# Performance work log

Hardware: AMD Instinct MI355X
Metric: run time of the kernel (lower is better)

Reference implementation:

```python
import jax, jax.numpy as jnp
import numpy as np

DIM = 256
HEADS = 8
PS = 8  # patch/window size
EPS = 1e-5


def _ln(x, g, b):
    m = x.mean(-1, keepdims=True)
    v = x.var(-1, keepdims=True)
    return (x - m) / jnp.sqrt(v + EPS) * g + b


def setup_inputs() -> dict:
    key = jax.random.key(0)
    ks = jax.random.split(key, 10)
    B, C, H, W = 4, DIM, 256, 256
    s = 0.02
    return {
        "y_lf": jax.random.normal(ks[0], (B, C, H, W), jnp.float32),
        "y_hf": jax.random.normal(ks[1], (B, C, H, W), jnp.float32),
        "g_lf": jnp.ones((C,), jnp.float32),
        "b_lf": jnp.zeros((C,), jnp.float32),
        "g_hf": jnp.ones((C,), jnp.float32),
        "b_hf": jnp.zeros((C,), jnp.float32),
        "Wq": jax.random.normal(ks[2], (C, C), jnp.float32) * s,
        "bq": jnp.zeros((C,), jnp.float32),
        "Wk": jax.random.normal(ks[3], (C, C), jnp.float32) * s,
        "bk": jnp.zeros((C,), jnp.float32),
        "Wv": jax.random.normal(ks[4], (C, C), jnp.float32) * s,
        "bv": jnp.zeros((C,), jnp.float32),
        "Wo": jax.random.normal(ks[5], (C, C), jnp.float32) * s,
        "bo": jnp.zeros((C,), jnp.float32),
    }


def reference(y_lf, y_hf, g_lf, b_lf, g_hf, b_hf, Wq, bq, Wk, bk, Wv, bv, Wo, bo):
    B, C, H, W = y_lf.shape
    ps = PS
    hd = C // HEADS
    nH, nW = H // ps, W // ps

    def win_tokens(x):
        # (B,C,H,W) -> (B*nH*nW, ps*ps, C)
        x = x.reshape(B, C, nH, ps, nW, ps)
        return x.transpose(0, 2, 4, 3, 5, 1).reshape(-1, ps * ps, C)

    lf = win_tokens(y_lf)
    hf = win_tokens(y_hf)  # residual + V source (un-normalized, as in torch code)

    q = _ln(lf, g_lf, b_lf) @ Wq.T + bq
    k = _ln(hf, g_hf, b_hf) @ Wk.T + bk
    v = hf @ Wv.T + bv

    BW, L, _ = q.shape
    q = q.reshape(BW, L, HEADS, hd)
    k = k.reshape(BW, L, HEADS, hd)
    v = v.reshape(BW, L, HEADS, hd)

    scale = 1.0 / np.sqrt(hd).astype(np.float32)
    scores = jnp.einsum('bqhd,bkhd->bhqk', q, k) * scale
    attn = jax.nn.softmax(scores, axis=-1)
    o = jnp.einsum('bhqk,bkhd->bqhd', attn, v).reshape(BW, L, C)
    o = o @ Wo.T + bo + hf  # out_proj + residual

    # window_reverse: (B*nH*nW, ps*ps, C) -> (B,C,H,W)
    o = o.reshape(B, nH, nW, ps, ps, C)
    o = o.transpose(0, 5, 1, 3, 2, 4).reshape(B, C, H, W)
    return o
```

## Files before the change

### kernel.cpp

```cpp
#include <hip/hip_runtime.h>

typedef float  f4     __attribute__((ext_vector_type(4)));
typedef float  f32x4  __attribute__((ext_vector_type(4)));
typedef short  short8 __attribute__((ext_vector_type(8)));
typedef __bf16 bf16x8 __attribute__((ext_vector_type(8)));
typedef int    int4v  __attribute__((ext_vector_type(4)));
typedef unsigned short us4 __attribute__((ext_vector_type(4)));

__device__ __forceinline__ unsigned short f2bf(float f) {
    unsigned int u = __builtin_bit_cast(unsigned int, f);
    u += 0x7FFFu + ((u >> 16) & 1u);
    return (unsigned short)(u >> 16);
}
__device__ __forceinline__ float bf2f(unsigned short h) {
    unsigned int u = ((unsigned int)h) << 16;
    return __builtin_bit_cast(float, u);
}
__device__ __forceinline__ f32x4 mfma_bf16(short8 a, short8 b, f32x4 c) {
    return __builtin_amdgcn_mfma_f32_16x16x32_bf16(
        __builtin_bit_cast(bf16x8, a), __builtin_bit_cast(bf16x8, b), c, 0, 0, 0);
}
__device__ __forceinline__ int cvt_pk_bf16(float lo, float hi) {
    int d;
    asm volatile("v_cvt_pk_bf16_f32 %0, %1, %2" : "=v"(d) : "v"(lo), "v"(hi));
    return d;
}
__device__ __forceinline__ int bperm(int addr, int src) {
    return __builtin_amdgcn_ds_bpermute(addr, src);
}

__global__ void pcaf_precvt(const float* __restrict__ Wq, const float* __restrict__ bq,
                            const float* __restrict__ Wk, const float* __restrict__ bk,
                            const float* __restrict__ Wv, const float* __restrict__ Wo,
                            const float* __restrict__ g_lf, const float* __restrict__ b_lf,
                            const float* __restrict__ g_hf, const float* __restrict__ b_hf,
                            void* __restrict__ ws) {
    const int mat  = blockIdx.x >> 8;
    const int row  = blockIdx.x & 255;
    const int lane = threadIdx.x;
    const float* W = (mat == 0) ? Wq : (mat == 1) ? Wk : (mat == 2) ? Wv : Wo;
    f4 w = *(const f4*)(W + row * 256 + lane * 4);
    f4 wp = w;
    if (mat < 2) {
        const float* g = mat ? g_hf : g_lf;
        f4 gg = *(const f4*)(g + lane * 4);
        wp = w * gg;
    }
    us4 u;
    u[0] = f2bf(wp[0]); u[1] = f2bf(wp[1]); u[2] = f2bf(wp[2]); u[3] = f2bf(wp[3]);
    *(us4*)((unsigned short*)ws + mat * 65536 + row * 256 + lane * 4) = u;
    if (mat < 2) {
        const float* b = mat ? b_hf : b_lf;
        f4 bb = *(const f4*)(b + lane * 4);
        float rsum = wp[0] + wp[1] + wp[2] + wp[3];
        float cb   = bb[0] * w[0] + bb[1] * w[1] + bb[2] * w[2] + bb[3] * w[3];
        #pragma unroll
        for (int d = 1; d < 64; d <<= 1) {
            rsum += __shfl_xor(rsum, d);
            cb   += __shfl_xor(cb, d);
        }
        if (lane == 0) {
            float* cons = (float*)((char*)ws + 524288);
            cons[mat * 512 + row]       = rsum;
            cons[mat * 512 + 256 + row] = cb + (mat ? bk[row] : bq[row]);
        }
    }
}

struct AccW { f32x4 a[4][2]; };

__device__ __forceinline__ AccW gemmW(const char* sm, int off,
                                      const unsigned short* __restrict__ Wb,
                                      int c0, int g, int l15) {
    AccW r;
    f32x4 z = {0.f, 0.f, 0.f, 0.f};
    #pragma unroll
    for (int m = 0; m < 4; ++m) { r.a[m][0] = z; r.a[m][1] = z; }
    #pragma unroll
    for (int half = 0; half < 2; ++half) {
        short8 w0[4], w1[4];
        #pragma unroll
        for (int k = 0; k < 4; ++k) {
            w0[k] = *(const short8*)(Wb + c0 * 256 + (half * 4 + k) * 32 + g * 8);
            w1[k] = *(const short8*)(Wb + (c0 + 16) * 256 + (half * 4 + k) * 32 + g * 8);
        }
        #pragma unroll
        for (int k = 0; k < 4; ++k) {
            #pragma unroll
            for (int m = 0; m < 4; ++m) {
                short8 am = *(const short8*)(sm + off + (16 * m + l15) * 528 +
                                             ((half * 4 + k) * 32 + g * 8) * 2);
                r.a[m][0] = mfma_bf16(am, w0[k], r.a[m][0]);
                r.a[m][1] = mfma_bf16(am, w1[k], r.a[m][1]);
            }
        }
    }
    return r;
}

__global__ __attribute__((amdgpu_flat_work_group_size(512, 512), amdgpu_waves_per_eu(4, 4)))
void pcaf4_kernel(
    const float* __restrict__ y_lf, const float* __restrict__ y_hf,
    const float* __restrict__ bv, const float* __restrict__ bo,
    const void* __restrict__ ws, float* __restrict__ out)
{
    constexpr int C = 256, H = 256, W = 256, HW = H * W;
    constexpr int RS = 528;
    constexpr int OA = 0;
    constexpr int OB = 33792;
    constexpr int OS = 67584;
    __shared__ __align__(16) char sm[68608];

    const unsigned short* wsq = (const unsigned short*)ws;
    const unsigned short* wsk = wsq + 65536;
    const unsigned short* wsv = wsq + 131072;
    const unsigned short* wso = wsq + 196608;
    const float* cons = (const float*)((const char*)ws + 524288);

    const int tid = threadIdx.x;
    const int bid = blockIdx.x;
    const int wi  = ((bid & 7) << 9) | (bid >> 3);
    const int bb  = wi >> 10;
    const int nh  = (wi >> 5) & 31;
    const int nw  = wi & 31;
    const long win_base = (long)bb * C * HW + (long)(nh * 8) * W + nw * 8;

    const int wave = tid >> 6;
    const int lane = tid & 63;
    const int g    = lane >> 4;
    const int l15  = lane & 15;
    const int c0   = 32 * wave + l15;

    {
        f4 lv[8], hv[8];
        #pragma unroll
        for (int it = 0; it < 4; ++it) {
            int q2  = it * 512 + tid;
            int c2  = q2 >> 4;
            int ph  = (q2 >> 1) & 7;
            int pw4 = (q2 & 1) * 4;
            long go = win_base + (long)(2 * c2) * HW + ph * W + pw4;
            lv[2 * it]     = *(const f4*)(y_lf + go);
            lv[2 * it + 1] = *(const f4*)(y_lf + go + HW);
            hv[2 * it]     = *(const f4*)(y_hf + go);
            hv[2 * it + 1] = *(const f4*)(y_hf + go + HW);
        }
        #pragma unroll
        for (int it = 0; it < 4; ++it) {
            int q2  = it * 512 + tid;
            int c2  = q2 >> 4;
            int ph  = (q2 >> 1) & 7;
            int pw4 = (q2 & 1) * 4;
            int tok0 = ph * 8 + pw4;
            #pragma unroll
            for (int j = 0; j < 4; ++j) {
                unsigned int lvv = (unsigned int)f2bf(lv[2 * it][j]) | ((unsigned int)f2bf(lv[2 * it + 1][j]) << 16);
                unsigned int hvv = (unsigned int)f2bf(hv[2 * it][j]) | ((unsigned int)f2bf(hv[2 * it + 1][j]) << 16);
                *(unsigned int*)(sm + OA + (tok0 + j) * RS + c2 * 4) = lvv;
                *(unsigned int*)(sm + OB + (tok0 + j) * RS + c2 * 4) = hvv;
            }
        }
    }
    __syncthreads();

    {
        const int t = tid >> 3, j = tid & 7;
        #pragma unroll
        for (int pass = 0; pass < 2; ++pass) {
            const int base = pass ? OB : OA;
            float sum = 0.f, ss = 0.f;
            #pragma unroll
            for (int r = 0; r < 4; ++r) {
                short8 raw = *(const short8*)(sm + base + t * RS + (j * 32 + r * 8) * 2);
                #pragma unroll
                for (int e = 0; e < 8; ++e) { float f = bf2f((unsigned short)raw[e]); sum += f; ss += f * f; }
            }
            sum += __shfl_xor(sum, 1); ss += __shfl_xor(ss, 1);
            sum += __shfl_xor(sum, 2); ss += __shfl_xor(ss, 2);
            sum += __shfl_xor(sum, 4); ss += __shfl_xor(ss, 4);
            float mean = sum * (1.f / 256.f);
            float rstd = rsqrtf(ss * (1.f / 256.f) - mean * mean + 1e-5f);
            if (j == 0) {
                float* S = (float*)(sm + OS);
                S[pass * 128 + t]      = mean;
                S[pass * 128 + 64 + t] = rstd;
            }
        }
    }

    AccW qacc = gemmW(sm, OA, wsq, c0, g, l15);

    unsigned int resp[4][2][2];
    #pragma unroll
    for (int m = 0; m < 4; ++m)
        #pragma unroll
        for (int n = 0; n < 2; ++n)
            #pragma unroll
            for (int jh = 0; jh < 2; ++jh) {
                unsigned int lo = *(const unsigned short*)(sm + OB + (16 * m + 4 * g + 2 * jh) * RS + (c0 + 16 * n) * 2);
                unsigned int hi = *(const unsigned short*)(sm + OB + (16 * m + 4 * g + 2 * jh + 1) * RS + (c0 + 16 * n) * 2);
                resp[m][n][jh] = lo | (hi << 16);
            }

    int vp[4][2][2];
    {
        AccW vacc = gemmW(sm, OB, wsv, c0, g, l15);
        float bv0 = bv[c0], bv1 = bv[c0 + 16];
        #pragma unroll
        for (int m = 0; m < 4; ++m) {
            vp[m][0][0] = cvt_pk_bf16(vacc.a[m][0][0] + bv0, vacc.a[m][0][1] + bv0);
            vp[m][0][1] = cvt_pk_bf16(vacc.a[m][0][2] + bv0, vacc.a[m][0][3] + bv0);
            vp[m][1][0] = cvt_pk_bf16(vacc.a[m][1][0] + bv1, vacc.a[m][1][1] + bv1);
            vp[m][1][1] = cvt_pk_bf16(vacc.a[m][1][2] + bv1, vacc.a[m][1][3] + bv1);
        }
    }
    __syncthreads();

    {
        const float* S = (const float*)(sm + OS);
        const float SCALE = 0.17677669529663687f;
        float rs0 = cons[c0], rs1 = cons[c0 + 16];
        float cb0 = cons[256 + c0], cb1 = cons[256 + c0 + 16];
        #pragma unroll
        for (int m = 0; m < 4; ++m)
            #pragma unroll
            for (int i = 0; i < 4; ++i) {
                int t = 16 * m + 4 * g + i;
                float mean = S[t], rstd = S[64 + t];
                float v0 = (rstd * (qacc.a[m][0][i] - mean * rs0) + cb0) * SCALE;
                float v1 = (rstd * (qacc.a[m][1][i] - mean * rs1) + cb1) * SCALE;
                *(unsigned short*)(sm + OA + t * RS + c0 * 2)        = f2bf(v0);
                *(unsigned short*)(sm + OA + t * RS + (c0 + 16) * 2) = f2bf(v1);
            }
    }

    AccW kacc = gemmW(sm, OB, wsk, c0, g, l15);
    __syncthreads();

    {
        const float* S = (const float*)(sm + OS);
        float rs0 = cons[512 + c0], rs1 = cons[512 + c0 + 16];
        float cb0 = cons[768 + c0], cb1 = cons[768 + c0 + 16];
        #pragma unroll
        for (int m = 0; m < 4; ++m)
            #pragma unroll
            for (int i = 0; i < 4; ++i) {
                int t = 16 * m + 4 * g + i;
                float mean = S[128 + t], rstd = S[192 + t];
                float v0 = rstd * (kacc.a[m][0][i] - mean * rs0) + cb0;
                float v1 = rstd * (kacc.a[m][1][i] - mean * rs1) + cb1;
                *(unsigned short*)(sm + OB + t * RS + c0 * 2)        = f2bf(v0);
                *(unsigned short*)(sm + OB + t * RS + (c0 + 16) * 2) = f2bf(v1);
            }
    }
    __syncthreads();

    {
        const int w = wave;
        short8 kf[4], qf[4];
        #pragma unroll
        for (int x = 0; x < 4; ++x) {
            kf[x] = *(const short8*)(sm + OB + (16 * x + l15) * RS + (32 * w + 8 * g) * 2);
            qf[x] = *(const short8*)(sm + OA + (16 * x + l15) * RS + (32 * w + 8 * g) * 2);
        }
        __syncthreads();

        f32x4 z = {0.f, 0.f, 0.f, 0.f};

        const int a0 = ((2 * (g & 1)) * 16 + l15) * 4;
        const int a1 = a0 + 64;
        const bool ghi = (g >> 1) & 1;

        short8 vf[2][2];
        #pragma unroll
        for (int kk = 0; kk < 2; ++kk)
            #pragma unroll
            for (int n2 = 0; n2 < 2; ++n2) {
                int4v t;
                #pragma unroll
                for (int j = 0; j < 4; ++j) {
                    int ad = (j >> 1) ? a1 : a0;
                    int v0 = bperm(ad, vp[2 * kk][n2][j & 1]);
                    int v1 = bperm(ad, vp[2 * kk + 1][n2][j & 1]);
                    t[j] = ghi ? v1 : v0;
                }
                vf[kk][n2] = __builtin_bit_cast(short8, t);
            }

        f32x4 o[4][2];
        #pragma unroll
        for (int c = 0; c < 4; ++c) { o[c][0] = z; o[c][1] = z; }

        #pragma unroll
        for (int c = 0; c < 4; ++c) {
            f32x4 stc[4];
            #pragma unroll
            for (int nk = 0; nk < 4; ++nk)
                stc[nk] = mfma_bf16(kf[nk], qf[c], z);

            float mx = stc[0][0];
            #pragma unroll
            for (int nk = 0; nk < 4; ++nk)
                #pragma unroll
                for (int i = 0; i < 4; ++i) mx = fmaxf(mx, stc[nk][i]);
            mx = fmaxf(mx, __shfl_xor(mx, 16));
            mx = fmaxf(mx, __shfl_xor(mx, 32));
            float sum = 0.f;
            #pragma unroll
            for (int nk = 0; nk < 4; ++nk)
                #pragma unroll
                for (int i = 0; i < 4; ++i) {
                    float e = __expf(stc[nk][i] - mx);
                    stc[nk][i] = e;
                    sum += e;
                }
            sum += __shfl_xor(sum, 16);
            sum += __shfl_xor(sum, 32);
            float is = 1.f / sum;

            int p[4][2];
            #pragma unroll
            for (int nk = 0; nk < 4; ++nk) {
                p[nk][0] = cvt_pk_bf16(stc[nk][0] * is, stc[nk][1] * is);
                p[nk][1] = cvt_pk_bf16(stc[nk][2] * is, stc[nk][3] * is);
            }

            #pragma unroll
            for (int kk = 0; kk < 2; ++kk) {
                int4v t;
                #pragma unroll
                for (int j = 0; j < 4; ++j) {
                    int ad = (j >> 1) ? a1 : a0;
                    int v0 = bperm(ad, p[2 * kk][j & 1]);
                    int v1 = bperm(ad, p[2 * kk + 1][j & 1]);
                    t[j] = ghi ? v1 : v0;
                }
                short8 pf = __builtin_bit_cast(short8, t);
                o[c][0] = mfma_bf16(pf, vf[kk][0], o[c][0]);
                o[c][1] = mfma_bf16(pf, vf[kk][1], o[c][1]);
            }
        }

        #pragma unroll
        for (int c = 0; c < 4; ++c)
            #pragma unroll
            for (int i = 0; i < 4; ++i) {
                int t = 16 * c + 4 * g + i;
                *(unsigned short*)(sm + OA + t * RS + c0 * 2)        = f2bf(o[c][0][i]);
                *(unsigned short*)(sm + OA + t * RS + (c0 + 16) * 2) = f2bf(o[c][1][i]);
            }
    }
    __syncthreads();

    {
        AccW oacc = gemmW(sm, OA, wso, c0, g, l15);
        float bo0 = bo[c0], bo1 = bo[c0 + 16];
        #pragma unroll
        for (int n = 0; n < 2; ++n) {
            float bon = n ? bo1 : bo0;
            int cout = c0 + 16 * n;
            #pragma unroll
            for (int m = 0; m < 4; ++m) {
                int tok0 = 16 * m + 4 * g;
                int ph = tok0 >> 3, pw = tok0 & 7;
                f4 ov;
                #pragma unroll
                for (int i = 0; i < 4; ++i) {
                    float rv = bf2f((unsigned short)((resp[m][n][i >> 1] >> (16 * (i & 1))) & 0xFFFF));
                    ov[i] = oacc.a[m][n][i] + bon + rv;
                }
                *(f4*)(out + win_base + (long)cout * HW + ph * W + pw) = ov;
            }
        }
    }
}

extern "C" void kernel_launch(void* const* d_in, const int* in_sizes, int n_in,
                              void* d_out, int out_size, void* d_ws, size_t ws_size,
                              hipStream_t stream) {
    (void)in_sizes; (void)n_in; (void)out_size; (void)ws_size;
    const float* y_lf = (const float*)d_in[0];
    const float* y_hf = (const float*)d_in[1];
    const float* g_lf = (const float*)d_in[2];
    const float* b_lf = (const float*)d_in[3];
    const float* g_hf = (const float*)d_in[4];
    const float* b_hf = (const float*)d_in[5];
    const float* Wq   = (const float*)d_in[6];
    const float* bq   = (const float*)d_in[7];
    const float* Wk   = (const float*)d_in[8];
    const float* bk   = (const float*)d_in[9];
    const float* Wv   = (const float*)d_in[10];
    const float* bv   = (const float*)d_in[11];
    const float* Wo   = (const float*)d_in[12];
    const float* bo   = (const float*)d_in[13];
    float* out = (float*)d_out;

    pcaf_precvt<<<dim3(1024), dim3(64), 0, stream>>>(
        Wq, bq, Wk, bk, Wv, Wo, g_lf, b_lf, g_hf, b_hf, d_ws);
    pcaf4_kernel<<<dim3(4096), dim3(512), 0, stream>>>(
        y_lf, y_hf, bv, bo, d_ws, out);
}
```

Before: 513.5 us.

## Pre-swizzle bf16 weights into MFMA fragment order and change LDS row stride

```diff
diff --git a/kernel.cpp b/kernel.cpp
--- a/kernel.cpp
+++ b/kernel.cpp
@@ -48,7 +48,16 @@
     }
     us4 u;
     u[0] = f2bf(wp[0]); u[1] = f2bf(wp[1]); u[2] = f2bf(wp[2]); u[3] = f2bf(wp[3]);
-    *(us4*)((unsigned short*)ws + mat * 65536 + row * 256 + lane * 4) = u;
+    {
+        const int ct   = row >> 4;
+        const int l15r = row & 15;
+        const int k_   = lane >> 3;
+        const int g_   = (lane >> 1) & 3;
+        const int e4   = (lane & 1) * 4;
+        unsigned short* dst = (unsigned short*)ws + mat * 65536 +
+                              (((ct * 8 + k_) * 64) + g_ * 16 + l15r) * 8 + e4;
+        *(us4*)dst = u;
+    }
     if (mat < 2) {
         const float* b = mat ? b_hf : b_lf;
         f4 bb = *(const f4*)(b + lane * 4);
@@ -67,11 +76,13 @@
     }
 }
 
+constexpr int RS = 536;
+
 struct AccW { f32x4 a[4][2]; };
 
 __device__ __forceinline__ AccW gemmW(const char* sm, int off,
-                                      const unsigned short* __restrict__ Wb,
-                                      int c0, int g, int l15) {
+                                      const unsigned short* __restrict__ Wbw,
+                                      int lane, int g, int l15) {
     AccW r;
     f32x4 z = {0.f, 0.f, 0.f, 0.f};
     #pragma unroll
@@ -81,14 +92,14 @@
         short8 w0[4], w1[4];
         #pragma unroll
         for (int k = 0; k < 4; ++k) {
-            w0[k] = *(const short8*)(Wb + c0 * 256 + (half * 4 + k) * 32 + g * 8);
-            w1[k] = *(const short8*)(Wb + (c0 + 16) * 256 + (half * 4 + k) * 32 + g * 8);
+            w0[k] = *(const short8*)(Wbw + (half * 4 + k) * 512 + lane * 8);
+            w1[k] = *(const short8*)(Wbw + 4096 + (half * 4 + k) * 512 + lane * 8);
         }
         #pragma unroll
         for (int k = 0; k < 4; ++k) {
             #pragma unroll
             for (int m = 0; m < 4; ++m) {
-                short8 am = *(const short8*)(sm + off + (16 * m + l15) * 528 +
+                short8 am = *(const short8*)(sm + off + (16 * m + l15) * RS +
                                              ((half * 4 + k) * 32 + g * 8) * 2);
                 r.a[m][0] = mfma_bf16(am, w0[k], r.a[m][0]);
                 r.a[m][1] = mfma_bf16(am, w1[k], r.a[m][1]);
@@ -99,17 +110,16 @@
 }
 
 __global__ __attribute__((amdgpu_flat_work_group_size(512, 512), amdgpu_waves_per_eu(4, 4)))
-void pcaf4_kernel(
+void pcaf5_kernel(
     const float* __restrict__ y_lf, const float* __restrict__ y_hf,
     const float* __restrict__ bv, const float* __restrict__ bo,
     const void* __restrict__ ws, float* __restrict__ out)
 {
     constexpr int C = 256, H = 256, W = 256, HW = H * W;
-    constexpr int RS = 528;
     constexpr int OA = 0;
-    constexpr int OB = 33792;
-    constexpr int OS = 67584;
-    __shared__ __align__(16) char sm[68608];
+    constexpr int OB = 34304;
+    constexpr int OS = 68608;
+    __shared__ __align__(16) char sm[69632];
 
     const unsigned short* wsq = (const unsigned short*)ws;
     const unsigned short* wsk = wsq + 65536;
@@ -188,7 +198,7 @@
         }
     }
 
-    AccW qacc = gemmW(sm, OA, wsq, c0, g, l15);
+    AccW qacc = gemmW(sm, OA, wsq + wave * 8192, lane, g, l15);
 
     unsigned int resp[4][2][2];
     #pragma unroll
@@ -204,7 +214,7 @@
 
     int vp[4][2][2];
     {
-        AccW vacc = gemmW(sm, OB, wsv, c0, g, l15);
+        AccW vacc = gemmW(sm, OB, wsv + wave * 8192, lane, g, l15);
         float bv0 = bv[c0], bv1 = bv[c0 + 16];
         #pragma unroll
         for (int m = 0; m < 4; ++m) {
@@ -234,7 +244,7 @@
             }
     }
 
-    AccW kacc = gemmW(sm, OB, wsk, c0, g, l15);
+    AccW kacc = gemmW(sm, OB, wsk + wave * 8192, lane, g, l15);
     __syncthreads();
 
     {
@@ -353,7 +363,7 @@
     __syncthreads();
 
     {
-        AccW oacc = gemmW(sm, OA, wso, c0, g, l15);
+        AccW oacc = gemmW(sm, OA, wso + wave * 8192, lane, g, l15);
         float bo0 = bo[c0], bo1 = bo[c0 + 16];
         #pragma unroll
         for (int n = 0; n < 2; ++n) {
@@ -397,6 +407,6 @@
 
     pcaf_precvt<<<dim3(1024), dim3(64), 0, stream>>>(
         Wq, bq, Wk, bk, Wv, Wo, g_lf, b_lf, g_hf, b_hf, d_ws);
-    pcaf4_kernel<<<dim3(4096), dim3(512), 0, stream>>>(
+    pcaf5_kernel<<<dim3(4096), dim3(512), 0, stream>>>(
         y_lf, y_hf, bv, bo, d_ws, out);
 }
```

Result: slower. 688.5 us (+34.1%).
